# Kernel tuning notes

Hardware: AMD Instinct MI355X
Metric: run time of the kernel (lower is better)

Reference implementation:

```python
import jax, jax.numpy as jnp
import numpy as np

B, N, D, H, F = 2, 2048, 512, 8, 2048
HD = D // H
EPS = 1e-5

def _ln(x, g, b):
    m = jnp.mean(x, axis=-1, keepdims=True)
    v = jnp.mean((x - m) ** 2, axis=-1, keepdims=True)
    return (x - m) * jax.lax.rsqrt(v + EPS) * g + b

def setup_inputs() -> dict:
    key = jax.random.key(0)
    ks = jax.random.split(key, 20)
    def lin(k, din, dout, std=0.05):
        kw, kb = jax.random.split(k)
        return (jax.random.normal(kw, (din, dout), jnp.float32) * std,
                jnp.zeros((dout,), jnp.float32))
    Wq, bq = lin(ks[0], D, D)
    Wk, bk = lin(ks[1], D, D)
    Wv, bv = lin(ks[2], D, D)
    Wg, bg = lin(ks[3], D, D)
    Wo, bo = lin(ks[4], D, D)
    W1, b1 = lin(ks[5], D, F)
    W2, b2 = lin(ks[6], F, D)
    return {
        'x': jax.random.normal(ks[7], (B, N, D), jnp.float32),
        'attn_bias': jax.random.normal(ks[8], (B, N, N, H), jnp.float32) * 0.1,
        'attn_mask': jnp.zeros((B, N, N), jnp.bool_),
        'Wq': Wq, 'bq': bq, 'Wk': Wk, 'bk': bk, 'Wv': Wv, 'bv': bv,
        'Wg': Wg, 'bg': bg, 'Wo': Wo, 'bo': bo,
        'ln1_g': jnp.ones((D,), jnp.float32), 'ln1_b': jnp.zeros((D,), jnp.float32),
        'ln2_g': jnp.ones((D,), jnp.float32), 'ln2_b': jnp.zeros((D,), jnp.float32),
        'W1': W1, 'b1': b1, 'W2': W2, 'b2': b2,
    }

def reference(x, attn_bias, attn_mask, Wq, bq, Wk, bk, Wv, bv, Wg, bg, Wo, bo,
              ln1_g, ln1_b, ln2_g, ln2_b, W1, b1, W2, b2):
    scaling = HD ** -0.5
    # --- self-attention sublayer (pre-LN) ---
    y = _ln(x, ln1_g, ln1_b)
    q = (y @ Wq + bq).reshape(B, N, H, HD) * scaling
    k = (y @ Wk + bk).reshape(B, N, H, HD)
    v = (y @ Wv + bv).reshape(B, N, H, HD)
    u = y * jax.nn.sigmoid(y @ Wg + bg)            # GLU gating branch
    scores = jnp.einsum('bqhd,bkhd->bqkh', q, k)   # [B, Nq, Nk, H]
    scores = scores + attn_bias                    # attn_bias_type == 'add'
    scores = jnp.where(attn_mask[..., None], -jnp.inf, scores)
    w = jax.nn.softmax(scores, axis=2)             # softmax over keys
    attn = jnp.einsum('bqkh,bkhd->bqhd', w, v).reshape(B, N, D)
    attn = attn @ Wo + bo
    y = u + attn
    x = x + y                                      # residual (dropout = identity, eval)
    # --- FFN sublayer (pre-LN) ---
    y = _ln(x, ln2_g, ln2_b)
    y = jax.nn.gelu(y @ W1 + b1, approximate=False) @ W2 + b2
    return x + y
```

## Files before the change

### kernel.cpp

```cpp
#include <hip/hip_runtime.h>
#include <hip/hip_bf16.h>

#define DI __device__ __forceinline__

typedef __attribute__((ext_vector_type(8))) __bf16 bf16x8;
typedef __attribute__((ext_vector_type(4))) float f32x4;
typedef __attribute__((ext_vector_type(4))) unsigned short u16x4;
typedef __attribute__((ext_vector_type(8))) unsigned short u16x8;

DI unsigned short f2bs(float f) {
  __hip_bfloat16 h = __float2bfloat16(f);
  return __builtin_bit_cast(unsigned short, h);
}
DI float bs2f(unsigned short s) {
  return __bfloat162float(__builtin_bit_cast(__hip_bfloat16, s));
}
DI f32x4 mfma16(bf16x8 a, bf16x8 b, f32x4 c) {
  return __builtin_amdgcn_mfma_f32_16x16x32_bf16(a, b, c, 0, 0, 0);
}
DI void g2lds16(const void* g, void* l) {
  __builtin_amdgcn_global_load_lds(
      (__attribute__((address_space(1))) void*)(unsigned long long)g,
      (__attribute__((address_space(3))) void*)l, 16, 0, 0);
}
#define SB __builtin_amdgcn_sched_barrier(0)
DI void barrier_lgkm() {
  asm volatile("s_waitcnt lgkmcnt(0)" ::: "memory");
  SB;
  __builtin_amdgcn_s_barrier();
  SB;
}
DI void vm_guard3() {
  SB;
  asm volatile("s_waitcnt vmcnt(3)" ::: "memory");
  SB;
}

__global__ __launch_bounds__(256) void k_transw(const float* __restrict__ W,
                                                unsigned short* __restrict__ Wt,
                                                int K, int N) {
  __shared__ float tile[64][65];
  int tk = blockIdx.x * 64, tn = blockIdx.y * 64;
  int t = threadIdx.x;
#pragma unroll
  for (int i = 0; i < 16; ++i) {
    int idx = t + i * 256;
    int r = idx >> 6, c = idx & 63;
    tile[r][c] = W[(size_t)(tk + r) * N + tn + c];
  }
  __syncthreads();
#pragma unroll
  for (int i = 0; i < 16; ++i) {
    int idx = t + i * 256;
    int n = idx >> 6, kk = idx & 63;
    Wt[(size_t)(tn + n) * K + tk + kk] = f2bs(tile[kk][n]);
  }
}

__global__ __launch_bounds__(256) void k_bcat(const float* __restrict__ bq,
                                              const float* __restrict__ bk,
                                              const float* __restrict__ bv,
                                              const float* __restrict__ bg,
                                              float* __restrict__ bcat) {
  int t = blockIdx.x * 256 + threadIdx.x;
  const float* src = t < 512 ? bq : t < 1024 ? bk : t < 1536 ? bv : bg;
  bcat[t] = src[t & 511];
}

__global__ __launch_bounds__(256) void k_ln(const float* __restrict__ x,
                                            const float* __restrict__ g,
                                            const float* __restrict__ b,
                                            unsigned short* __restrict__ y) {
  int row = blockIdx.x, t = threadIdx.x;
  const float* xr = x + (size_t)row * 512;
  float a0 = xr[t], a1 = xr[t + 256];
  float s1 = a0 + a1, s2 = a0 * a0 + a1 * a1;
#pragma unroll
  for (int o = 32; o > 0; o >>= 1) {
    s1 += __shfl_down(s1, o);
    s2 += __shfl_down(s2, o);
  }
  __shared__ float r1[4], r2[4], bc[2];
  int w = t >> 6, l = t & 63;
  if (l == 0) { r1[w] = s1; r2[w] = s2; }
  __syncthreads();
  if (t == 0) {
    float t1 = r1[0] + r1[1] + r1[2] + r1[3];
    float t2 = r2[0] + r2[1] + r2[2] + r2[3];
    float m = t1 / 512.f;
    float v = t2 / 512.f - m * m;
    bc[0] = m;
    bc[1] = rsqrtf(v + 1e-5f);
  }
  __syncthreads();
  float m = bc[0], inv = bc[1];
  y[(size_t)row * 512 + t] = f2bs((a0 - m) * inv * g[t] + b[t]);
  y[(size_t)row * 512 + t + 256] = f2bs((a1 - m) * inv * g[t + 256] + b[t + 256]);
}

template <int BM>
__global__ __launch_bounds__(256) void k_gemm(
    const unsigned short* __restrict__ A, const unsigned short* __restrict__ Bt,
    const float* __restrict__ bias, int M, int N, int K, int mode,
    float* __restrict__ outf, unsigned short* __restrict__ outh,
    const float* __restrict__ add1, const float* __restrict__ add2,
    unsigned short* __restrict__ vtout) {
  constexpr int MI = BM / 32;
  __shared__ __align__(16) unsigned short lA[BM * 64];
  __shared__ __align__(16) unsigned short lB[64 * 64];
  int t = threadIdx.x, w = t >> 6, l = t & 63;
  int l15 = l & 15, lg = l >> 4;
  int m0 = blockIdx.x * BM, n0 = blockIdx.y * 64;
  int wm = (w >> 1) * (BM / 2), wn = (w & 1) * 32;
  f32x4 acc[MI][2] = {};
  int sr = l >> 3, scb = (l & 7) * 16;
  for (int k0 = 0; k0 < K; k0 += 64) {
#pragma unroll
    for (int c = 0; c < MI; ++c) {
      int row = w * (BM / 4) + sr + c * 8;
      g2lds16((const char*)A + ((size_t)(m0 + row) * K + k0) * 2 + scb,
              (char*)lA + w * (BM / 4) * 128 + c * 1024);
    }
#pragma unroll
    for (int c = 0; c < 2; ++c) {
      int row = w * 16 + sr + c * 8;
      g2lds16((const char*)Bt + ((size_t)(n0 + row) * K + k0) * 2 + scb,
              (char*)lB + w * 2048 + c * 1024);
    }
    __syncthreads();
#pragma unroll
    for (int kc = 0; kc < 2; ++kc) {
      bf16x8 af[MI], bfr[2];
#pragma unroll
      for (int i = 0; i < MI; ++i)
        af[i] = *(const bf16x8*)((const char*)lA + (wm + i * 16 + l15) * 128 + kc * 64 + lg * 16);
#pragma unroll
      for (int j = 0; j < 2; ++j)
        bfr[j] = *(const bf16x8*)((const char*)lB + (wn + j * 16 + l15) * 128 + kc * 64 + lg * 16);
#pragma unroll
      for (int i = 0; i < MI; ++i)
#pragma unroll
        for (int j = 0; j < 2; ++j)
          acc[i][j] = mfma16(af[i], bfr[j], acc[i][j]);
    }
    __syncthreads();
  }
#pragma unroll
  for (int i = 0; i < MI; ++i) {
#pragma unroll
    for (int j = 0; j < 2; ++j) {
      int col = n0 + wn + j * 16 + l15;
      int row0 = m0 + wm + i * 16 + lg * 4;
      float vals[4];
#pragma unroll
      for (int r = 0; r < 4; ++r) vals[r] = acc[i][j][r] + bias[col];
      if (mode == 6) {
        int sel = col >> 9, c5 = col & 511;
        if (sel == 2) {
          int hh = c5 >> 6, dd = c5 & 63, bb = row0 >> 11, nn = row0 & 2047;
          u16x4 pk;
#pragma unroll
          for (int r = 0; r < 4; ++r) pk[r] = f2bs(vals[r]);
          *(u16x4*)(vtout + (((size_t)(bb * 8 + hh) * 64 + dd) * 2048 + nn)) = pk;
        } else {
#pragma unroll
          for (int r = 0; r < 4; ++r) {
            size_t idx = (size_t)(row0 + r) * 512 + c5;
            if (sel == 0) outh[idx] = f2bs(vals[r] * 0.125f);
            else if (sel == 1) outh[2097152 + idx] = f2bs(vals[r]);
            else outf[idx] = bs2f(A[idx]) * (1.f / (1.f + __expf(-vals[r])));
          }
        }
      } else {
#pragma unroll
        for (int r = 0; r < 4; ++r) {
          size_t idx = (size_t)(row0 + r) * N + col;
          if (mode == 3) outf[idx] = vals[r] + add1[idx] + add2[idx];
          else if (mode == 4) outh[idx] = f2bs(0.5f * vals[r] * (1.f + erff(vals[r] * 0.70710678f)));
          else outf[idx] = vals[r] + add1[idx];
        }
      }
    }
  }
}

__global__ __launch_bounds__(512, 1) void k_attn14(
    const unsigned short* __restrict__ q, const unsigned short* __restrict__ kk,
    const unsigned short* __restrict__ vt, const float* __restrict__ bias,
    const unsigned char* __restrict__ mask, unsigned short* __restrict__ ao) {
  __shared__ __align__(16) char lsK[2][32768];
  __shared__ __align__(16) char lsV[2][32768];
  __shared__ __align__(16) char lsB[2][16 * 520];
  __shared__ __align__(16) unsigned short ls_p[8][16][36];

  int bid = blockIdx.x;
  int b = bid >> 7, qt = bid & 127;
  int q0 = qt * 16;
  int t = threadIdx.x, w = t >> 6, l = t & 63;
  int l15 = l & 15, lg = l >> 4;
  int h = w;

  bf16x8 qa0 = *(const bf16x8*)(q + ((size_t)(b * 2048 + q0 + l15) * 512 + h * 64 + lg * 8));
  bf16x8 qa1 = *(const bf16x8*)(q + ((size_t)(b * 2048 + q0 + l15) * 512 + h * 64 + 32 + lg * 8));

  union { bf16x8 v; unsigned short s[8]; } uo;
#pragma unroll
  for (int j = 0; j < 8; ++j) uo.s[j] = 0x3F80;
  const bf16x8 vones = uo.v;

  f32x4 oacc[4] = {};
  f32x4 lacc = {};

  const char* kptr[4];
  char* kdst[4];
#pragma unroll
  for (int i = 0; i < 4; ++i) {
    int fi = t + i * 512;
    int row = fi >> 6;
    int colb = ((fi & 63) * 16) ^ ((row & 7) << 4);
    kptr[i] = (const char*)kk + ((size_t)(b * 2048 + row) * 512) * 2 + colb;
    kdst[i] = (char*)0 + (i * 512 + w * 64) * 16;
  }
  const char* vptr[4];
#pragma unroll
  for (int i = 0; i < 4; ++i) {
    int fi = t + i * 512;
    int rv = fi >> 2;
    int dv = rv & 63, hv = rv >> 6;
    int slot = (fi & 3) ^ (dv & 3);
    vptr[i] = (const char*)vt + (((size_t)(b * 8 + hv) * 64 + dv) * 2048 + slot * 8) * 2;
  }
  int qq = t >> 5, kc = t & 31;
  const float* bptr = bias + ((size_t)(b * 2048 + q0 + qq) * 2048 + kc) * 8;
  const unsigned char* mptr = mask + (size_t)(b * 2048 + q0 + qq) * 2048 + kc;
  char* bdst = (char*)0 + qq * 520 + kc * 16;
  const unsigned short BN = f2bs(-1e30f);

#define STAGEKV(buf, kb)                                                     \
  do {                                                                       \
    _Pragma("unroll") for (int i = 0; i < 4; ++i)                            \
        g2lds16(kptr[i] + (size_t)(kb) * 1024, lsK[buf] + (size_t)kdst[i]);  \
    _Pragma("unroll") for (int i = 0; i < 4; ++i)                            \
        g2lds16(vptr[i] + (size_t)(kb) * 2, lsV[buf] + (size_t)kdst[i]);     \
  } while (0)
#define LOADB(BA, BB, MB, kb)                                                \
  do {                                                                       \
    BA = *(const float4*)(bptr + (size_t)(kb) * 8);                          \
    BB = *(const float4*)(bptr + (size_t)(kb) * 8 + 4);                      \
    MB = mptr[kb];                                                           \
  } while (0)
#define WRITEB(buf, BA, BB, MB)                                              \
  do {                                                                       \
    u16x8 o;                                                                 \
    if (MB) {                                                                \
      _Pragma("unroll") for (int j = 0; j < 8; ++j) o[j] = BN;               \
    } else {                                                                 \
      o[0] = f2bs(BA.x); o[1] = f2bs(BA.y); o[2] = f2bs(BA.z);               \
      o[3] = f2bs(BA.w); o[4] = f2bs(BB.x); o[5] = f2bs(BB.y);               \
      o[6] = f2bs(BB.z); o[7] = f2bs(BB.w);                                  \
    }                                                                        \
    *(u16x8*)(lsB[buf] + (size_t)bdst) = o;                                  \
  } while (0)
#define LDSK(buf, tt, kcc)                                                   \
  (*(const bf16x8*)(lsK[buf] + ((tt)*16 + l15) * 1024 +                      \
                    ((h * 128 + (kcc)*64 + lg * 16) ^ ((((tt)*16 + l15) & 7) << 4))))
#define LDSV(buf, dt)                                                        \
  (*(const bf16x8*)(lsV[buf] +                                               \
                    (((h * 64 + (dt)*16 + l15) * 4 +                         \
                      (lg ^ (((dt)*16 + l15) & 3))) * 16)))
#define COMPUTE(buf)                                                         \
  do {                                                                       \
    f32x4 sc0 = {}, sc1 = {};                                                \
    sc0 = mfma16(qa0, LDSK(buf, 0, 0), sc0);                                 \
    sc0 = mfma16(qa1, LDSK(buf, 0, 1), sc0);                                 \
    sc1 = mfma16(qa0, LDSK(buf, 1, 0), sc1);                                 \
    sc1 = mfma16(qa1, LDSK(buf, 1, 1), sc1);                                 \
    _Pragma("unroll") for (int r = 0; r < 4; ++r) {                          \
      int qr = lg * 4 + r;                                                   \
      float b0 = bs2f(*(const unsigned short*)(lsB[buf] + qr * 520 + l15 * 16 + h * 2));          \
      float b1 = bs2f(*(const unsigned short*)(lsB[buf] + qr * 520 + (l15 + 16) * 16 + h * 2));   \
      float p0 = __expf(sc0[r] + b0 - 8.0f);                                 \
      float p1 = __expf(sc1[r] + b1 - 8.0f);                                 \
      ls_p[w][qr][l15] = f2bs(p0);                                           \
      ls_p[w][qr][16 + l15] = f2bs(p1);                                      \
    }                                                                        \
    bf16x8 pa = *(const bf16x8*)&ls_p[w][l15][lg * 8];                       \
    oacc[0] = mfma16(pa, LDSV(buf, 0), oacc[0]);                             \
    oacc[1] = mfma16(pa, LDSV(buf, 1), oacc[1]);                             \
    oacc[2] = mfma16(pa, LDSV(buf, 2), oacc[2]);                             \
    oacc[3] = mfma16(pa, LDSV(buf, 3), oacc[3]);                             \
    lacc = mfma16(pa, vones, lacc);                                          \
  } while (0)

  float4 rA0, rA1, rB0, rB1;
  unsigned char mA, mB;
  LOADB(rA0, rA1, mA, 0);
  WRITEB(0, rA0, rA1, mA);
  LOADB(rB0, rB1, mB, 32);
  SB;
  STAGEKV(0, 0);
  SB;
  vm_guard3();
  barrier_lgkm();
  for (int it = 0; it < 64; it += 2) {
    int kb1 = (it + 1) * 32;
    int kb2 = (it + 2 < 64) ? (it + 2) * 32 : 0;
    int kb3 = (it + 3 < 64) ? (it + 3) * 32 : 0;
    SB;
    STAGEKV(1, kb1);
    SB;
    LOADB(rA0, rA1, mA, kb2);
    SB;
    COMPUTE(0);
    WRITEB(1, rB0, rB1, mB);
    vm_guard3();
    barrier_lgkm();
    SB;
    STAGEKV(0, kb2);
    SB;
    LOADB(rB0, rB1, mB, kb3);
    SB;
    COMPUTE(1);
    WRITEB(0, rA0, rA1, mA);
    vm_guard3();
    barrier_lgkm();
  }
#undef STAGEKV
#undef LOADB
#undef WRITEB
#undef LDSK
#undef LDSV
#undef COMPUTE

#pragma unroll
  for (int d = 0; d < 4; ++d)
#pragma unroll
    for (int r = 0; r < 4; ++r) {
      size_t row = (size_t)(b * 2048 + q0 + lg * 4 + r);
      ao[row * 512 + h * 64 + d * 16 + l15] = f2bs(oacc[d][r] / lacc[r]);
    }
}

extern "C" void kernel_launch(void* const* d_in, const int* in_sizes, int n_in,
                              void* d_out, int out_size, void* d_ws, size_t ws_size,
                              hipStream_t stream) {
  (void)in_sizes; (void)n_in; (void)out_size; (void)ws_size;
  const float* x = (const float*)d_in[0];
  const float* abias = (const float*)d_in[1];
  const unsigned char* amask = (const unsigned char*)d_in[2];
  const float* Wq = (const float*)d_in[3];
  const float* bq = (const float*)d_in[4];
  const float* Wk = (const float*)d_in[5];
  const float* bk = (const float*)d_in[6];
  const float* Wv = (const float*)d_in[7];
  const float* bv = (const float*)d_in[8];
  const float* Wg = (const float*)d_in[9];
  const float* bg = (const float*)d_in[10];
  const float* Wo = (const float*)d_in[11];
  const float* bo = (const float*)d_in[12];
  const float* ln1g = (const float*)d_in[13];
  const float* ln1b = (const float*)d_in[14];
  const float* ln2g = (const float*)d_in[15];
  const float* ln2b = (const float*)d_in[16];
  const float* W1 = (const float*)d_in[17];
  const float* b1 = (const float*)d_in[18];
  const float* W2 = (const float*)d_in[19];
  const float* b2 = (const float*)d_in[20];
  float* outp = (float*)d_out;

  char* ws = (char*)d_ws;
  const size_t MB = 1024 * 1024;

  unsigned short* qb = (unsigned short*)(ws + 0);
  unsigned short* kb = (unsigned short*)(ws + 4 * MB);
  unsigned short* ao = (unsigned short*)(ws + 8 * MB);
  unsigned short* y1 = (unsigned short*)(ws + 28 * MB);
  unsigned short* h1 = (unsigned short*)(ws + 0);
  float* u = (float*)(ws + 32 * MB);
  unsigned short* wcat = (unsigned short*)(ws + 40 * MB);
  unsigned short* wot = (unsigned short*)(ws + 42 * MB);
  unsigned short* w1t = (unsigned short*)(ws + 42 * MB + 512 * 1024);
  unsigned short* w2t = (unsigned short*)(ws + 44 * MB + 512 * 1024);
  float* bcat = (float*)(ws + 46 * MB + 512 * 1024);
  unsigned short* vtb = (unsigned short*)(ws + 48 * MB);
  float* x2 = (float*)d_out;

  k_transw<<<dim3(8, 8), 256, 0, stream>>>(Wq, wcat + 0 * 512 * 512, 512, 512);
  k_transw<<<dim3(8, 8), 256, 0, stream>>>(Wk, wcat + 1 * 512 * 512, 512, 512);
  k_transw<<<dim3(8, 8), 256, 0, stream>>>(Wv, wcat + 2 * 512 * 512, 512, 512);
  k_transw<<<dim3(8, 8), 256, 0, stream>>>(Wg, wcat + 3 * 512 * 512, 512, 512);
  k_transw<<<dim3(8, 8), 256, 0, stream>>>(Wo, wot, 512, 512);
  k_transw<<<dim3(8, 32), 256, 0, stream>>>(W1, w1t, 512, 2048);
  k_transw<<<dim3(32, 8), 256, 0, stream>>>(W2, w2t, 2048, 512);
  k_bcat<<<8, 256, 0, stream>>>(bq, bk, bv, bg, bcat);

  k_ln<<<4096, 256, 0, stream>>>(x, ln1g, ln1b, y1);
  k_gemm<128><<<dim3(32, 32), 256, 0, stream>>>(y1, wcat, bcat, 4096, 2048, 512, 6,
                                                u, qb, nullptr, nullptr, vtb);
  k_attn14<<<256, 512, 0, stream>>>(qb, kb, vtb, abias, amask, ao);
  k_gemm<64><<<dim3(64, 8), 256, 0, stream>>>(ao, wot, bo, 4096, 512, 512, 3,
                                              x2, nullptr, u, x, nullptr);
  k_ln<<<4096, 256, 0, stream>>>(x2, ln2g, ln2b, y1);
  k_gemm<128><<<dim3(32, 32), 256, 0, stream>>>(y1, w1t, b1, 4096, 2048, 512, 4,
                                                nullptr, h1, nullptr, nullptr, nullptr);
  k_gemm<64><<<dim3(64, 8), 256, 0, stream>>>(h1, w2t, b2, 4096, 512, 2048, 5,
                                              outp, nullptr, x2, nullptr, nullptr);
}
```

Measured before the change: 269.0 us.

## Use 128x128 GEMM tiles everywhere and pad attention bias LDS layout

Replaces the templated GEMM (128x64 or 64x64 tiles) with a single 128x128 tile kernel in which each wave computes a 64x64 sub-tile (4x4 MFMA fragments), raising data reuse per LDS load. The small N=512 GEMMs now launch only 128 blocks, which may underfill the GPU. The attention kernel changes the bias staging LDS layout to a 648-byte row pitch and 20-byte per-key stride, written as four 32-bit stores, to reduce bank conflicts on the per-head bias reads.

```diff
diff --git a/kernel.cpp b/kernel.cpp
--- a/kernel.cpp
+++ b/kernel.cpp
@@ -98,57 +98,51 @@
   y[(size_t)row * 512 + t + 256] = f2bs((a1 - m) * inv * g[t + 256] + b[t + 256]);
 }
 
-template <int BM>
-__global__ __launch_bounds__(256) void k_gemm(
+__global__ __launch_bounds__(256) void k_gemm2(
     const unsigned short* __restrict__ A, const unsigned short* __restrict__ Bt,
     const float* __restrict__ bias, int M, int N, int K, int mode,
     float* __restrict__ outf, unsigned short* __restrict__ outh,
     const float* __restrict__ add1, const float* __restrict__ add2,
     unsigned short* __restrict__ vtout) {
-  constexpr int MI = BM / 32;
-  __shared__ __align__(16) unsigned short lA[BM * 64];
-  __shared__ __align__(16) unsigned short lB[64 * 64];
+  __shared__ __align__(16) unsigned short lA[128 * 64];
+  __shared__ __align__(16) unsigned short lB[128 * 64];
   int t = threadIdx.x, w = t >> 6, l = t & 63;
   int l15 = l & 15, lg = l >> 4;
-  int m0 = blockIdx.x * BM, n0 = blockIdx.y * 64;
-  int wm = (w >> 1) * (BM / 2), wn = (w & 1) * 32;
-  f32x4 acc[MI][2] = {};
-  int sr = l >> 3, scb = (l & 7) * 16;
+  int m0 = blockIdx.x * 128, n0 = blockIdx.y * 128;
+  int wm = (w >> 1) * 64, wn = (w & 1) * 64;
+  f32x4 acc[4][4] = {};
+  int srow = w * 32 + (l >> 3);
+  int scolb = (l & 7) * 16;
   for (int k0 = 0; k0 < K; k0 += 64) {
 #pragma unroll
-    for (int c = 0; c < MI; ++c) {
-      int row = w * (BM / 4) + sr + c * 8;
-      g2lds16((const char*)A + ((size_t)(m0 + row) * K + k0) * 2 + scb,
-              (char*)lA + w * (BM / 4) * 128 + c * 1024);
-    }
-#pragma unroll
-    for (int c = 0; c < 2; ++c) {
-      int row = w * 16 + sr + c * 8;
-      g2lds16((const char*)Bt + ((size_t)(n0 + row) * K + k0) * 2 + scb,
-              (char*)lB + w * 2048 + c * 1024);
+    for (int c = 0; c < 4; ++c) {
+      int row = srow + c * 8;
+      g2lds16((const char*)A + ((size_t)(m0 + row) * K + k0) * 2 + scolb,
+              (char*)lA + w * 4096 + c * 1024);
+      g2lds16((const char*)Bt + ((size_t)(n0 + row) * K + k0) * 2 + scolb,
+              (char*)lB + w * 4096 + c * 1024);
     }
     __syncthreads();
 #pragma unroll
     for (int kc = 0; kc < 2; ++kc) {
-      bf16x8 af[MI], bfr[2];
-#pragma unroll
-      for (int i = 0; i < MI; ++i)
+      bf16x8 af[4], bfr[4];
+#pragma unroll
+      for (int i = 0; i < 4; ++i) {
         af[i] = *(const bf16x8*)((const char*)lA + (wm + i * 16 + l15) * 128 + kc * 64 + lg * 16);
-#pragma unroll
-      for (int j = 0; j < 2; ++j)
-        bfr[j] = *(const bf16x8*)((const char*)lB + (wn + j * 16 + l15) * 128 + kc * 64 + lg * 16);
-#pragma unroll
-      for (int i = 0; i < MI; ++i)
-#pragma unroll
-        for (int j = 0; j < 2; ++j)
+        bfr[i] = *(const bf16x8*)((const char*)lB + (wn + i * 16 + l15) * 128 + kc * 64 + lg * 16);
+      }
+#pragma unroll
+      for (int i = 0; i < 4; ++i)
+#pragma unroll
+        for (int j = 0; j < 4; ++j)
           acc[i][j] = mfma16(af[i], bfr[j], acc[i][j]);
     }
     __syncthreads();
   }
 #pragma unroll
-  for (int i = 0; i < MI; ++i) {
-#pragma unroll
-    for (int j = 0; j < 2; ++j) {
+  for (int i = 0; i < 4; ++i) {
+#pragma unroll
+    for (int j = 0; j < 4; ++j) {
       int col = n0 + wn + j * 16 + l15;
       int row0 = m0 + wm + i * 16 + lg * 4;
       float vals[4];
@@ -184,13 +178,15 @@
   }
 }
 
-__global__ __launch_bounds__(512, 1) void k_attn14(
+#define BPITCH 648
+#define KSTR 20
+__global__ __launch_bounds__(512, 1) void k_attn15(
     const unsigned short* __restrict__ q, const unsigned short* __restrict__ kk,
     const unsigned short* __restrict__ vt, const float* __restrict__ bias,
     const unsigned char* __restrict__ mask, unsigned short* __restrict__ ao) {
   __shared__ __align__(16) char lsK[2][32768];
   __shared__ __align__(16) char lsV[2][32768];
-  __shared__ __align__(16) char lsB[2][16 * 520];
+  __shared__ __align__(16) char lsB[2][16 * BPITCH];
   __shared__ __align__(16) unsigned short ls_p[8][16][36];
 
   int bid = blockIdx.x;
@@ -233,7 +229,7 @@
   int qq = t >> 5, kc = t & 31;
   const float* bptr = bias + ((size_t)(b * 2048 + q0 + qq) * 2048 + kc) * 8;
   const unsigned char* mptr = mask + (size_t)(b * 2048 + q0 + qq) * 2048 + kc;
-  char* bdst = (char*)0 + qq * 520 + kc * 16;
+  char* bdst = (char*)0 + qq * BPITCH + kc * KSTR;
   const unsigned short BN = f2bs(-1e30f);
 
 #define STAGEKV(buf, kb)                                                     \
@@ -251,15 +247,17 @@
   } while (0)
 #define WRITEB(buf, BA, BB, MB)                                              \
   do {                                                                       \
-    u16x8 o;                                                                 \
+    unsigned d0, d1, d2, d3;                                                 \
     if (MB) {                                                                \
-      _Pragma("unroll") for (int j = 0; j < 8; ++j) o[j] = BN;               \
+      d0 = d1 = d2 = d3 = ((unsigned)BN << 16) | BN;                         \
     } else {                                                                 \
-      o[0] = f2bs(BA.x); o[1] = f2bs(BA.y); o[2] = f2bs(BA.z);               \
-      o[3] = f2bs(BA.w); o[4] = f2bs(BB.x); o[5] = f2bs(BB.y);               \
-      o[6] = f2bs(BB.z); o[7] = f2bs(BB.w);                                  \
+      d0 = f2bs(BA.x) | ((unsigned)f2bs(BA.y) << 16);                        \
+      d1 = f2bs(BA.z) | ((unsigned)f2bs(BA.w) << 16);                        \
+      d2 = f2bs(BB.x) | ((unsigned)f2bs(BB.y) << 16);                        \
+      d3 = f2bs(BB.z) | ((unsigned)f2bs(BB.w) << 16);                        \
     }                                                                        \
-    *(u16x8*)(lsB[buf] + (size_t)bdst) = o;                                  \
+    unsigned* bp_ = (unsigned*)(lsB[buf] + (size_t)bdst);                    \
+    bp_[0] = d0; bp_[1] = d1; bp_[2] = d2; bp_[3] = d3;                      \
   } while (0)
 #define LDSK(buf, tt, kcc)                                                   \
   (*(const bf16x8*)(lsK[buf] + ((tt)*16 + l15) * 1024 +                      \
@@ -277,8 +275,8 @@
     sc1 = mfma16(qa1, LDSK(buf, 1, 1), sc1);                                 \
     _Pragma("unroll") for (int r = 0; r < 4; ++r) {                          \
       int qr = lg * 4 + r;                                                   \
-      float b0 = bs2f(*(const unsigned short*)(lsB[buf] + qr * 520 + l15 * 16 + h * 2));          \
-      float b1 = bs2f(*(const unsigned short*)(lsB[buf] + qr * 520 + (l15 + 16) * 16 + h * 2));   \
+      float b0 = bs2f(*(const unsigned short*)(lsB[buf] + qr * BPITCH + l15 * KSTR + h * 2));        \
+      float b1 = bs2f(*(const unsigned short*)(lsB[buf] + qr * BPITCH + (l15 + 16) * KSTR + h * 2)); \
       float p0 = __expf(sc0[r] + b0 - 8.0f);                                 \
       float p1 = __expf(sc1[r] + b1 - 8.0f);                                 \
       ls_p[w][qr][l15] = f2bs(p0);                                           \
@@ -395,14 +393,14 @@
   k_bcat<<<8, 256, 0, stream>>>(bq, bk, bv, bg, bcat);
 
   k_ln<<<4096, 256, 0, stream>>>(x, ln1g, ln1b, y1);
-  k_gemm<128><<<dim3(32, 32), 256, 0, stream>>>(y1, wcat, bcat, 4096, 2048, 512, 6,
-                                                u, qb, nullptr, nullptr, vtb);
-  k_attn14<<<256, 512, 0, stream>>>(qb, kb, vtb, abias, amask, ao);
-  k_gemm<64><<<dim3(64, 8), 256, 0, stream>>>(ao, wot, bo, 4096, 512, 512, 3,
-                                              x2, nullptr, u, x, nullptr);
+  k_gemm2<<<dim3(32, 16), 256, 0, stream>>>(y1, wcat, bcat, 4096, 2048, 512, 6,
+                                            u, qb, nullptr, nullptr, vtb);
+  k_attn15<<<256, 512, 0, stream>>>(qb, kb, vtb, abias, amask, ao);
+  k_gemm2<<<dim3(32, 4), 256, 0, stream>>>(ao, wot, bo, 4096, 512, 512, 3,
+                                           x2, nullptr, u, x, nullptr);
   k_ln<<<4096, 256, 0, stream>>>(x2, ln2g, ln2b, y1);
-  k_gemm<128><<<dim3(32, 32), 256, 0, stream>>>(y1, w1t, b1, 4096, 2048, 512, 4,
-                                                nullptr, h1, nullptr, nullptr, nullptr);
-  k_gemm<64><<<dim3(64, 8), 256, 0, stream>>>(h1, w2t, b2, 4096, 512, 2048, 5,
-                                              outp, nullptr, x2, nullptr, nullptr);
-}
+  k_gemm2<<<dim3(32, 16), 256, 0, stream>>>(y1, w1t, b1, 4096, 2048, 512, 4,
+                                            nullptr, h1, nullptr, nullptr, nullptr);
+  k_gemm2<<<dim3(32, 4), 256, 0, stream>>>(h1, w2t, b2, 4096, 512, 2048, 5,
+                                           outp, nullptr, x2, nullptr, nullptr);
+}
```

New measurement: 336.6 us. 25.2% more time.
